# Kernel tuning notes

Measured on AMD Instinct MI355X. Metric: run time of the kernel, lower is better.

Reference implementation:

```python
import jax, jax.numpy as jnp
import numpy as np

B, T, E, H = 4, 2048, 1024, 16
S = E // H  # 64


def setup_inputs() -> dict:
    key = jax.random.key(0)
    ks = jax.random.split(key, 6)
    return {
        "x": jax.random.normal(ks[0], (B, T, E), dtype=jnp.float32),
        "Wk": jax.random.normal(ks[1], (S, S), dtype=jnp.float32) * (1.0 / np.sqrt(S)),
        "Wq": jax.random.normal(ks[2], (S, S), dtype=jnp.float32) * (1.0 / np.sqrt(S)),
        "Wv": jax.random.normal(ks[3], (S, S), dtype=jnp.float32) * (1.0 / np.sqrt(S)),
        "Wp": jax.random.normal(ks[4], (E, E), dtype=jnp.float32) * (1.0 / np.sqrt(E)),
        "bp": jnp.zeros((E,), dtype=jnp.float32),
    }


def reference(x, Wk, Wq, Wv, Wp, bp):
    b, t, e = x.shape
    h, s = H, S
    xh = x.reshape(b, t, h, s)
    # per-head projections share one (s,s) weight across all heads (torch Linear: y = x @ W.T)
    keys = jnp.einsum('bthi,oi->bhto', xh, Wk)     # (b,h,t,s)
    queries = jnp.einsum('bthi,oi->bhto', xh, Wq)
    values = jnp.einsum('bthi,oi->bhto', xh, Wv)
    scale = e ** 0.25  # q and k each divided by e^(1/4) -> net 1/sqrt(e)
    queries = queries / scale
    keys = keys / scale
    dot = jnp.einsum('bhqs,bhks->bhqk', queries, keys)  # (b,h,t,t)
    attn = jax.nn.softmax(dot, axis=-1)
    out = jnp.einsum('bhqk,bhks->bqhs', attn, values)   # (b,t,h,s)
    out = out.reshape(b, t, h * s)
    return jnp.einsum('bte,oe->bto', out, Wp) + bp
```

## Files before the change

kernel.cpp:

```cpp
#include <hip/hip_runtime.h>
#include <hip/hip_bf16.h>

#define Bv 4
#define Tv 2048
#define Ev 1024
#define Hv 16
#define Sv 64

typedef __attribute__((ext_vector_type(8))) short bf16x8;
typedef __attribute__((ext_vector_type(4))) short bf16x4;
typedef __attribute__((ext_vector_type(4))) float f32x4;
typedef __attribute__((ext_vector_type(16))) float f32x16;

__device__ __forceinline__ ushort f2bf(float f) {
    unsigned u = __float_as_uint(f);
    u = (u + 0x7FFFu + ((u >> 16) & 1u)) >> 16;
    return (ushort)u;
}
__device__ __forceinline__ unsigned pkrn(float a, float b) {
    __hip_bfloat162 t = __float22bfloat162_rn(make_float2(a, b));
    unsigned r; __builtin_memcpy(&r, &t, 4); return r;
}
__device__ __forceinline__ unsigned pktr(float a, float b) {
    return __builtin_amdgcn_perm(__float_as_uint(b), __float_as_uint(a), 0x07060302u);
}

__device__ __forceinline__ void async16(void* lds, const void* g) {
    __builtin_amdgcn_global_load_lds(
        (const __attribute__((address_space(1))) unsigned int*)g,
        (__attribute__((address_space(3))) unsigned int*)lds, 16, 0, 0);
}

__global__ __launch_bounds__(256) void cast_kernel(
    const float* __restrict__ Wp, const float* __restrict__ Wq,
    const float* __restrict__ Wk, const float* __restrict__ Wv,
    ushort* __restrict__ Wpb, ushort* __restrict__ Wqb,
    ushort* __restrict__ Wkb, ushort* __restrict__ Wvb)
{
    int blk = blockIdx.x;
    if (blk < 1024) {
        int i = (blk * 256 + threadIdx.x) * 4;
        float4 v = *(const float4*)(Wp + i);
        uint2 o = {pkrn(v.x, v.y), pkrn(v.z, v.w)};
        *(uint2*)(Wpb + i) = o;
    } else {
        int p = blk - 1024;
        const float* src = (p == 0) ? Wq : ((p == 1) ? Wk : Wv);
        ushort* dst      = (p == 0) ? Wqb : ((p == 1) ? Wkb : Wvb);
        const float scale = (p == 0) ? 0.03125f * 1.4426950408889634f : 1.0f;
        #pragma unroll
        for (int it = 0; it < 4; ++it) {
            int i = (it * 256 + threadIdx.x) * 4;
            float4 v = *(const float4*)(src + i);
            uint2 o = {pkrn(v.x * scale, v.y * scale), pkrn(v.z * scale, v.w * scale)};
            *(uint2*)(dst + i) = o;
        }
    }
}

__global__ __launch_bounds__(192) void qkv_kernel(
    const float* __restrict__ x,
    const ushort* __restrict__ Wqb, const ushort* __restrict__ Wkb,
    const ushort* __restrict__ Wvb,
    ushort* __restrict__ Q, ushort* __restrict__ K, ushort* __restrict__ Vt)
{
    const int tid  = threadIdx.x;
    const int wave = tid >> 6;
    const int lane = tid & 63;
    const int m    = lane & 15;
    const int quad = lane >> 4;

    const ushort* Wsel = (wave == 0) ? Wqb : ((wave == 1) ? Wkb : Wvb);
    bf16x8 wf[4][2];
    #pragma unroll
    for (int ot = 0; ot < 4; ++ot)
        #pragma unroll
        for (int ks = 0; ks < 2; ++ks)
            wf[ot][ks] = *(const bf16x8*)&Wsel[(ot * 16 + m) * 64 + ks * 32 + quad * 8];

    const int tt = blockIdx.x >> 2;
    const int hg = blockIdx.x & 3;
    const int g0 = tt * 16;
    const int gm = g0 + m;
    const int b  = g0 >> 11;
    const int t0 = g0 & 2047;

    #pragma unroll
    for (int hi = 0; hi < 4; ++hi) {
        const int h  = hg * 4 + hi;
        const int bh = b * Hv + h;

        bf16x8 xf[2];
        #pragma unroll
        for (int ks = 0; ks < 2; ++ks) {
            const float* src = x + (size_t)gm * Ev + h * Sv + ks * 32 + quad * 8;
            float4 v0 = *(const float4*)src;
            float4 v1 = *(const float4*)(src + 4);
            unsigned pk[4];
            pk[0] = pkrn(v0.x, v0.y); pk[1] = pkrn(v0.z, v0.w);
            pk[2] = pkrn(v1.x, v1.y); pk[3] = pkrn(v1.z, v1.w);
            xf[ks] = *(bf16x8*)pk;
        }

        f32x4 acc[4];
        #pragma unroll
        for (int ot = 0; ot < 4; ++ot) acc[ot] = (f32x4){0.f, 0.f, 0.f, 0.f};

        if (wave < 2) {
            #pragma unroll
            for (int ks = 0; ks < 2; ++ks)
                #pragma unroll
                for (int ot = 0; ot < 4; ++ot)
                    acc[ot] = __builtin_amdgcn_mfma_f32_16x16x32_bf16(
                        wf[ot][ks], xf[ks], acc[ot], 0, 0, 0);
            ushort* dst = ((wave == 0) ? Q : K)
                        + ((size_t)bh * Tv + t0 + m) * Sv + quad * 4;
            #pragma unroll
            for (int ot = 0; ot < 4; ++ot) {
                uint2 w = {pkrn(acc[ot][0], acc[ot][1]), pkrn(acc[ot][2], acc[ot][3])};
                *(uint2*)(dst + ot * 16) = w;
            }
        } else {
            #pragma unroll
            for (int ks = 0; ks < 2; ++ks)
                #pragma unroll
                for (int st = 0; st < 4; ++st)
                    acc[st] = __builtin_amdgcn_mfma_f32_16x16x32_bf16(
                        xf[ks], wf[st][ks], acc[st], 0, 0, 0);
            ushort* vr = Vt + ((size_t)bh * Sv + m) * Tv + t0 + quad * 4;
            #pragma unroll
            for (int st = 0; st < 4; ++st) {
                uint2 w = {pkrn(acc[st][0], acc[st][1]), pkrn(acc[st][2], acc[st][3])};
                *(uint2*)(vr + (size_t)st * 16 * Tv) = w;
            }
        }
    }
}

__global__ __launch_bounds__(256, 2) void attn_kernel(
    const ushort* __restrict__ Q, const ushort* __restrict__ K,
    const ushort* __restrict__ Vt, ushort* __restrict__ O)
{
    __shared__ ushort kl[64 * 64];
    __shared__ ushort vl[64 * 64];
    __shared__ float  ll[4][64];

    const int tid  = threadIdx.x;
    const int wave = tid >> 6;
    const int lane = tid & 63;
    const int r31  = lane & 31;
    const int hi   = lane >> 5;
    const int bh   = blockIdx.x & 63;
    const int q0   = (blockIdx.x >> 6) << 8;

    const ushort* Qb = Q + ((size_t)bh * Tv + q0 + wave * 64 + r31) * Sv + hi * 8;
    bf16x8 qf[2][4];
    #pragma unroll
    for (int g = 0; g < 2; ++g)
        #pragma unroll
        for (int ks = 0; ks < 4; ++ks)
            qf[g][ks] = *(const bf16x8*)(Qb + (size_t)g * 32 * Sv + ks * 16);

    f32x16 oa[2][2];
    #pragma unroll
    for (int g = 0; g < 2; ++g)
        #pragma unroll
        for (int st = 0; st < 2; ++st)
            #pragma unroll
            for (int r = 0; r < 16; ++r)
                oa[g][st][r] = 0.f;
    float lsum[2] = {0.f, 0.f};

    const ushort* Kb = K  + (size_t)bh * Tv * Sv;
    const ushort* Vb = Vt + (size_t)bh * Sv * Tv;

    const int r0 = tid >> 3,         cg0 = (tid & 7) ^ (r0 & 7);
    const int r1 = (256 + tid) >> 3, cg1 = ((256 + tid) & 7) ^ (r1 & 7);
    const size_t koff0 = (size_t)r0 * Sv + cg0 * 8;
    const size_t koff1 = (size_t)r1 * Sv + cg1 * 8;
    const size_t voff0 = (size_t)r0 * Tv + cg0 * 8;
    const size_t voff1 = (size_t)r1 * Tv + cg1 * 8;
    const int swz = r31 & 7;

    auto softpv = [&](const f32x16& sv, float& ls, f32x16* oag, int kp,
                      const bf16x8* vf) {
        float p[8];
        #pragma unroll
        for (int j = 0; j < 8; ++j)
            p[j] = __builtin_amdgcn_exp2f(sv[kp * 8 + j]);
        ls += ((p[0] + p[1]) + (p[2] + p[3]))
            + ((p[4] + p[5]) + (p[6] + p[7]));
        unsigned d0 = pktr(p[0], p[1]);
        unsigned d1 = pktr(p[2], p[3]);
        unsigned d2 = pktr(p[4], p[5]);
        unsigned d3 = pktr(p[6], p[7]);
        asm volatile("v_permlane32_swap_b32 %0, %1" : "+v"(d0), "+v"(d2));
        asm volatile("v_permlane32_swap_b32 %0, %1" : "+v"(d1), "+v"(d3));
        unsigned pw[4] = {d0, d1, d2, d3};
        bf16x8 pf = *(bf16x8*)pw;
        #pragma unroll
        for (int st = 0; st < 2; ++st)
            oag[st] = __builtin_amdgcn_mfma_f32_32x32x16_bf16(
                pf, vf[st], oag[st], 0, 0, 0);
    };

    for (int k0 = 0; k0 < Tv; k0 += 64) {
        __syncthreads();
        async16(&kl[(size_t)tid * 8],         Kb + (size_t)k0 * Sv + koff0);
        async16(&kl[((size_t)tid + 256) * 8], Kb + (size_t)k0 * Sv + koff1);
        async16(&vl[(size_t)tid * 8],         Vb + k0 + voff0);
        async16(&vl[((size_t)tid + 256) * 8], Vb + k0 + voff1);
        __syncthreads();

        #pragma unroll
        for (int kt = 0; kt < 2; ++kt) {
            bf16x8 kf[4];
            #pragma unroll
            for (int ks = 0; ks < 4; ++ks)
                kf[ks] = *(const bf16x8*)
                    &kl[(kt * 32 + r31) * 64 + (((ks * 2 + hi) ^ swz) * 8)];

            f32x16 s0, s1;
            #pragma unroll
            for (int r = 0; r < 16; ++r) { s0[r] = 0.f; s1[r] = 0.f; }
            #pragma unroll
            for (int ks = 0; ks < 4; ++ks)
                s0 = __builtin_amdgcn_mfma_f32_32x32x16_bf16(
                    kf[ks], qf[0][ks], s0, 0, 0, 0);
            #pragma unroll
            for (int ks = 0; ks < 4; ++ks)
                s1 = __builtin_amdgcn_mfma_f32_32x32x16_bf16(
                    kf[ks], qf[1][ks], s1, 0, 0, 0);

            #pragma unroll
            for (int kp = 0; kp < 2; ++kp) {
                const int kc = (kt * 2 + kp) * 2 + hi;
                bf16x8 vf[2];
                #pragma unroll
                for (int st = 0; st < 2; ++st)
                    vf[st] = *(const bf16x8*)
                        &vl[(st * 32 + r31) * 64 + ((kc ^ swz) * 8)];
                softpv(s0, lsum[0], oa[0], kp, vf);
                softpv(s1, lsum[1], oa[1], kp, vf);
            }
        }
    }

    lsum[0] += __shfl_xor(lsum[0], 32, 64);
    lsum[1] += __shfl_xor(lsum[1], 32, 64);
    if (hi == 0) {
        ll[wave][r31]      = 1.0f / lsum[0];
        ll[wave][32 + r31] = 1.0f / lsum[1];
    }

    const int b = bh >> 4, h = bh & 15;
    #pragma unroll
    for (int g = 0; g < 2; ++g) {
        float sc[16];
        #pragma unroll
        for (int r = 0; r < 16; ++r)
            sc[r] = ll[wave][g * 32 + (r & 3) + 4 * hi + 8 * (r >> 2)];
        #pragma unroll
        for (int st = 0; st < 2; ++st)
            #pragma unroll
            for (int r = 0; r < 16; ++r) {
                const int q = (r & 3) + 4 * hi + 8 * (r >> 2);
                O[((size_t)(b * Tv + q0 + wave * 64 + g * 32 + q)) * Ev
                  + h * Sv + st * 32 + r31] = f2bf(oa[g][st][r] * sc[r]);
            }
    }
}

__global__ __launch_bounds__(256) void proj_kernel(
    const ushort* __restrict__ A, const ushort* __restrict__ B,
    const float* __restrict__ bp, float* __restrict__ C)
{
    __shared__ ushort Asm[128 * 32];
    __shared__ ushort Bsm[128 * 32];
    const int tid  = threadIdx.x;
    const int wave = tid >> 6;
    const int lane = tid & 63;
    const int m    = lane & 15;
    const int quad = lane >> 4;
    const int wm   = wave >> 1;
    const int wn   = wave & 1;
    const int m0   = blockIdx.x * 128;
    const int n0   = blockIdx.y * 128;

    f32x4 acc[4][4];
    #pragma unroll
    for (int i = 0; i < 4; ++i)
        #pragma unroll
        for (int j = 0; j < 4; ++j)
            acc[i][j] = (f32x4){0.f, 0.f, 0.f, 0.f};

    for (int k0 = 0; k0 < Ev; k0 += 32) {
        __syncthreads();
        #pragma unroll
        for (int j = 0; j < 2; ++j) {
            int c   = j * 256 + tid;
            int row = c >> 2;
            int col = (c & 3) * 8;
            async16(&Asm[c * 8], &A[(size_t)(m0 + row) * Ev + k0 + col]);
            async16(&Bsm[c * 8], &B[(size_t)(n0 + row) * Ev + k0 + col]);
        }
        __syncthreads();

        bf16x8 af[4], bf[4];
        #pragma unroll
        for (int i = 0; i < 4; ++i)
            af[i] = *(const bf16x8*)&Asm[(wm * 64 + i * 16 + m) * 32 + quad * 8];
        #pragma unroll
        for (int j = 0; j < 4; ++j)
            bf[j] = *(const bf16x8*)&Bsm[(wn * 64 + j * 16 + m) * 32 + quad * 8];
        #pragma unroll
        for (int i = 0; i < 4; ++i)
            #pragma unroll
            for (int j = 0; j < 4; ++j)
                acc[i][j] = __builtin_amdgcn_mfma_f32_16x16x32_bf16(
                    af[i], bf[j], acc[i][j], 0, 0, 0);
    }

    float bbv[4];
    #pragma unroll
    for (int j = 0; j < 4; ++j)
        bbv[j] = bp[n0 + wn * 64 + j * 16 + m];

    #pragma unroll
    for (int i = 0; i < 4; ++i)
        #pragma unroll
        for (int j = 0; j < 4; ++j)
            #pragma unroll
            for (int r = 0; r < 4; ++r)
                C[(size_t)(m0 + wm * 64 + i * 16 + quad * 4 + r) * Ev
                  + n0 + wn * 64 + j * 16 + m] = acc[i][j][r] + bbv[j];
}

extern "C" void kernel_launch(void* const* d_in, const int* in_sizes, int n_in,
                              void* d_out, int out_size, void* d_ws, size_t ws_size,
                              hipStream_t stream) {
    const float* x  = (const float*)d_in[0];
    const float* Wk = (const float*)d_in[1];
    const float* Wq = (const float*)d_in[2];
    const float* Wv = (const float*)d_in[3];
    const float* Wp = (const float*)d_in[4];
    const float* bp = (const float*)d_in[5];
    float* out = (float*)d_out;

    ushort* Q   = (ushort*)d_ws;
    ushort* K   = Q   + 8388608;
    ushort* Vt  = K   + 8388608;
    ushort* O   = Vt  + 8388608;
    ushort* Wpb = O   + 8388608;
    ushort* Wqb = Wpb + 1048576;
    ushort* Wkb = Wqb + 4096;
    ushort* Wvb = Wkb + 4096;

    cast_kernel<<<1027, 256, 0, stream>>>(Wp, Wq, Wk, Wv, Wpb, Wqb, Wkb, Wvb);
    qkv_kernel<<<2048, 192, 0, stream>>>(x, Wqb, Wkb, Wvb, Q, K, Vt);
    attn_kernel<<<512, 256, 0, stream>>>(Q, K, Vt, O);
    proj_kernel<<<dim3(64, 8), 256, 0, stream>>>(O, Wpb, bp, out);
}
```

Baseline: 218.2 us.

## Fuse weight casts into consumers and register-prefetch K/V into 4-slot LDS ring

Removes the separate weight-cast kernel. The QKV weights are now converted to bf16 (with the query scale) inside qkv_kernel, and Wp is converted on the fly while loading the proj_kernel B tile. The attention kernel replaces the per-64-key async load with two syncs by a register-prefetched 4-buffer LDS ring that handles two subtiles per iteration with one barrier. This saves a kernel launch and halves the attention barriers, but proj_kernel now reads fp32 Wp and repeats the conversion in every block, and attention LDS use grows fourfold, which may reduce occupancy.

```diff
diff --git a/kernel.cpp b/kernel.cpp
--- a/kernel.cpp
+++ b/kernel.cpp
@@ -8,7 +8,6 @@
 #define Sv 64
 
 typedef __attribute__((ext_vector_type(8))) short bf16x8;
-typedef __attribute__((ext_vector_type(4))) short bf16x4;
 typedef __attribute__((ext_vector_type(4))) float f32x4;
 typedef __attribute__((ext_vector_type(16))) float f32x16;
 
@@ -31,37 +30,10 @@
         (__attribute__((address_space(3))) unsigned int*)lds, 16, 0, 0);
 }
 
-__global__ __launch_bounds__(256) void cast_kernel(
-    const float* __restrict__ Wp, const float* __restrict__ Wq,
-    const float* __restrict__ Wk, const float* __restrict__ Wv,
-    ushort* __restrict__ Wpb, ushort* __restrict__ Wqb,
-    ushort* __restrict__ Wkb, ushort* __restrict__ Wvb)
-{
-    int blk = blockIdx.x;
-    if (blk < 1024) {
-        int i = (blk * 256 + threadIdx.x) * 4;
-        float4 v = *(const float4*)(Wp + i);
-        uint2 o = {pkrn(v.x, v.y), pkrn(v.z, v.w)};
-        *(uint2*)(Wpb + i) = o;
-    } else {
-        int p = blk - 1024;
-        const float* src = (p == 0) ? Wq : ((p == 1) ? Wk : Wv);
-        ushort* dst      = (p == 0) ? Wqb : ((p == 1) ? Wkb : Wvb);
-        const float scale = (p == 0) ? 0.03125f * 1.4426950408889634f : 1.0f;
-        #pragma unroll
-        for (int it = 0; it < 4; ++it) {
-            int i = (it * 256 + threadIdx.x) * 4;
-            float4 v = *(const float4*)(src + i);
-            uint2 o = {pkrn(v.x * scale, v.y * scale), pkrn(v.z * scale, v.w * scale)};
-            *(uint2*)(dst + i) = o;
-        }
-    }
-}
-
 __global__ __launch_bounds__(192) void qkv_kernel(
     const float* __restrict__ x,
-    const ushort* __restrict__ Wqb, const ushort* __restrict__ Wkb,
-    const ushort* __restrict__ Wvb,
+    const float* __restrict__ Wq, const float* __restrict__ Wk,
+    const float* __restrict__ Wv,
     ushort* __restrict__ Q, ushort* __restrict__ K, ushort* __restrict__ Vt)
 {
     const int tid  = threadIdx.x;
@@ -70,13 +42,23 @@
     const int m    = lane & 15;
     const int quad = lane >> 4;
 
-    const ushort* Wsel = (wave == 0) ? Wqb : ((wave == 1) ? Wkb : Wvb);
+    const float* Wsel = (wave == 0) ? Wq : ((wave == 1) ? Wk : Wv);
+    const float wscale = (wave == 0) ? 0.03125f * 1.4426950408889634f : 1.0f;
     bf16x8 wf[4][2];
     #pragma unroll
     for (int ot = 0; ot < 4; ++ot)
         #pragma unroll
-        for (int ks = 0; ks < 2; ++ks)
-            wf[ot][ks] = *(const bf16x8*)&Wsel[(ot * 16 + m) * 64 + ks * 32 + quad * 8];
+        for (int ks = 0; ks < 2; ++ks) {
+            const float* ws = &Wsel[(ot * 16 + m) * 64 + ks * 32 + quad * 8];
+            float4 w0 = *(const float4*)ws;
+            float4 w1 = *(const float4*)(ws + 4);
+            unsigned pk[4];
+            pk[0] = pkrn(w0.x * wscale, w0.y * wscale);
+            pk[1] = pkrn(w0.z * wscale, w0.w * wscale);
+            pk[2] = pkrn(w1.x * wscale, w1.y * wscale);
+            pk[3] = pkrn(w1.z * wscale, w1.w * wscale);
+            wf[ot][ks] = *(bf16x8*)pk;
+        }
 
     const int tt = blockIdx.x >> 2;
     const int hg = blockIdx.x & 3;
@@ -141,8 +123,8 @@
     const ushort* __restrict__ Q, const ushort* __restrict__ K,
     const ushort* __restrict__ Vt, ushort* __restrict__ O)
 {
-    __shared__ ushort kl[64 * 64];
-    __shared__ ushort vl[64 * 64];
+    __shared__ ushort kl[4][64 * 64];
+    __shared__ ushort vl[4][64 * 64];
     __shared__ float  ll[4][64];
 
     const int tid  = threadIdx.x;
@@ -204,21 +186,14 @@
                 pf, vf[st], oag[st], 0, 0, 0);
     };
 
-    for (int k0 = 0; k0 < Tv; k0 += 64) {
-        __syncthreads();
-        async16(&kl[(size_t)tid * 8],         Kb + (size_t)k0 * Sv + koff0);
-        async16(&kl[((size_t)tid + 256) * 8], Kb + (size_t)k0 * Sv + koff1);
-        async16(&vl[(size_t)tid * 8],         Vb + k0 + voff0);
-        async16(&vl[((size_t)tid + 256) * 8], Vb + k0 + voff1);
-        __syncthreads();
-
+    auto subtile = [&](const ushort* kbuf, const ushort* vbuf) {
         #pragma unroll
         for (int kt = 0; kt < 2; ++kt) {
             bf16x8 kf[4];
             #pragma unroll
             for (int ks = 0; ks < 4; ++ks)
                 kf[ks] = *(const bf16x8*)
-                    &kl[(kt * 32 + r31) * 64 + (((ks * 2 + hi) ^ swz) * 8)];
+                    &kbuf[(kt * 32 + r31) * 64 + (((ks * 2 + hi) ^ swz) * 8)];
 
             f32x16 s0, s1;
             #pragma unroll
@@ -239,11 +214,67 @@
                 #pragma unroll
                 for (int st = 0; st < 2; ++st)
                     vf[st] = *(const bf16x8*)
-                        &vl[(st * 32 + r31) * 64 + ((kc ^ swz) * 8)];
+                        &vbuf[(st * 32 + r31) * 64 + ((kc ^ swz) * 8)];
                 softpv(s0, lsum[0], oa[0], kp, vf);
                 softpv(s1, lsum[1], oa[1], kp, vf);
             }
         }
+    };
+
+    uint4 ka0, ka1, va0, va1, kb0, kb1, vb0, vb1;
+    ka0 = *(const uint4*)(Kb + koff0);
+    ka1 = *(const uint4*)(Kb + koff1);
+    va0 = *(const uint4*)(Vb + voff0);
+    va1 = *(const uint4*)(Vb + voff1);
+    *(uint4*)&kl[0][(size_t)tid * 8]         = ka0;
+    *(uint4*)&kl[0][((size_t)tid + 256) * 8] = ka1;
+    *(uint4*)&vl[0][(size_t)tid * 8]         = va0;
+    *(uint4*)&vl[0][((size_t)tid + 256) * 8] = va1;
+    ka0 = *(const uint4*)(Kb + (size_t)64 * Sv + koff0);
+    ka1 = *(const uint4*)(Kb + (size_t)64 * Sv + koff1);
+    va0 = *(const uint4*)(Vb + 64 + voff0);
+    va1 = *(const uint4*)(Vb + 64 + voff1);
+    *(uint4*)&kl[1][(size_t)tid * 8]         = ka0;
+    *(uint4*)&kl[1][((size_t)tid + 256) * 8] = ka1;
+    *(uint4*)&vl[1][(size_t)tid * 8]         = va0;
+    *(uint4*)&vl[1][((size_t)tid + 256) * 8] = va1;
+    ka0 = *(const uint4*)(Kb + (size_t)128 * Sv + koff0);
+    ka1 = *(const uint4*)(Kb + (size_t)128 * Sv + koff1);
+    va0 = *(const uint4*)(Vb + 128 + voff0);
+    va1 = *(const uint4*)(Vb + 128 + voff1);
+    kb0 = *(const uint4*)(Kb + (size_t)192 * Sv + koff0);
+    kb1 = *(const uint4*)(Kb + (size_t)192 * Sv + koff1);
+    vb0 = *(const uint4*)(Vb + 192 + voff0);
+    vb1 = *(const uint4*)(Vb + 192 + voff1);
+    __syncthreads();
+
+    for (int it = 0; it < 16; ++it) {
+        if (it < 15) {
+            const int w0 = (2 * it + 2) & 3, w1 = (2 * it + 3) & 3;
+            *(uint4*)&kl[w0][(size_t)tid * 8]         = ka0;
+            *(uint4*)&kl[w0][((size_t)tid + 256) * 8] = ka1;
+            *(uint4*)&vl[w0][(size_t)tid * 8]         = va0;
+            *(uint4*)&vl[w0][((size_t)tid + 256) * 8] = va1;
+            *(uint4*)&kl[w1][(size_t)tid * 8]         = kb0;
+            *(uint4*)&kl[w1][((size_t)tid + 256) * 8] = kb1;
+            *(uint4*)&vl[w1][(size_t)tid * 8]         = vb0;
+            *(uint4*)&vl[w1][((size_t)tid + 256) * 8] = vb1;
+            int t4 = 2 * it + 4; if (t4 > 31) t4 = 0;
+            int t5 = 2 * it + 5; if (t5 > 31) t5 = 0;
+            ka0 = *(const uint4*)(Kb + (size_t)(t4 * 64) * Sv + koff0);
+            ka1 = *(const uint4*)(Kb + (size_t)(t4 * 64) * Sv + koff1);
+            va0 = *(const uint4*)(Vb + t4 * 64 + voff0);
+            va1 = *(const uint4*)(Vb + t4 * 64 + voff1);
+            kb0 = *(const uint4*)(Kb + (size_t)(t5 * 64) * Sv + koff0);
+            kb1 = *(const uint4*)(Kb + (size_t)(t5 * 64) * Sv + koff1);
+            vb0 = *(const uint4*)(Vb + t5 * 64 + voff0);
+            vb1 = *(const uint4*)(Vb + t5 * 64 + voff1);
+        }
+
+        subtile(kl[(2 * it) & 3],     vl[(2 * it) & 3]);
+        subtile(kl[(2 * it + 1) & 3], vl[(2 * it + 1) & 3]);
+
+        __syncthreads();
     }
 
     lsum[0] += __shfl_xor(lsum[0], 32, 64);
@@ -272,7 +303,7 @@
 }
 
 __global__ __launch_bounds__(256) void proj_kernel(
-    const ushort* __restrict__ A, const ushort* __restrict__ B,
+    const ushort* __restrict__ A, const float* __restrict__ Wp,
     const float* __restrict__ bp, float* __restrict__ C)
 {
     __shared__ ushort Asm[128 * 32];
@@ -301,8 +332,14 @@
             int c   = j * 256 + tid;
             int row = c >> 2;
             int col = (c & 3) * 8;
+            const float* wsrc = &Wp[(size_t)(n0 + row) * Ev + k0 + col];
+            float4 b0 = *(const float4*)wsrc;
+            float4 b1 = *(const float4*)(wsrc + 4);
             async16(&Asm[c * 8], &A[(size_t)(m0 + row) * Ev + k0 + col]);
-            async16(&Bsm[c * 8], &B[(size_t)(n0 + row) * Ev + k0 + col]);
+            unsigned pw[4];
+            pw[0] = pkrn(b0.x, b0.y); pw[1] = pkrn(b0.z, b0.w);
+            pw[2] = pkrn(b1.x, b1.y); pw[3] = pkrn(b1.z, b1.w);
+            *(uint4*)&Bsm[c * 8] = *(uint4*)pw;
         }
         __syncthreads();
 
@@ -351,13 +388,8 @@
     ushort* K   = Q   + 8388608;
     ushort* Vt  = K   + 8388608;
     ushort* O   = Vt  + 8388608;
-    ushort* Wpb = O   + 8388608;
-    ushort* Wqb = Wpb + 1048576;
-    ushort* Wkb = Wqb + 4096;
-    ushort* Wvb = Wkb + 4096;
-
-    cast_kernel<<<1027, 256, 0, stream>>>(Wp, Wq, Wk, Wv, Wpb, Wqb, Wkb, Wvb);
-    qkv_kernel<<<2048, 192, 0, stream>>>(x, Wqb, Wkb, Wvb, Q, K, Vt);
+
+    qkv_kernel<<<2048, 192, 0, stream>>>(x, Wq, Wk, Wv, Q, K, Vt);
     attn_kernel<<<512, 256, 0, stream>>>(Q, K, Vt, O);
-    proj_kernel<<<dim3(64, 8), 256, 0, stream>>>(O, Wpb, bp, out);
-}
+    proj_kernel<<<dim3(64, 8), 256, 0, stream>>>(O, Wp, bp, out);
+}
```

Measured after the change: 227.3 us. +4.2%, slower.
